# Kernel tuning notes

Measured on AMD Instinct MI355X. Metric: run time of the kernel, lower is better.

Reference implementation:

```python
import jax, jax.numpy as jnp
import numpy as np

EPS = 1e-5

def conv3x3(x, w, b):
    # x: [B,C,H,W], w: [O,I,3,3]
    y = jax.lax.conv_general_dilated(x, w, window_strides=(1, 1),
                                     padding=((1, 1), (1, 1)),
                                     dimension_numbers=('NCHW', 'OIHW', 'NCHW'))
    return y + b[None, :, None, None]

def batchnorm(x, gamma, beta):
    # training-mode BN: batch stats over (N,H,W), biased variance
    mean = jnp.mean(x, axis=(0, 2, 3), keepdims=True)
    var = jnp.mean((x - mean) ** 2, axis=(0, 2, 3), keepdims=True)
    xn = (x - mean) * jax.lax.rsqrt(var + EPS)
    return xn * gamma[None, :, None, None] + beta[None, :, None, None]

def setup_inputs() -> dict:
    key = jax.random.key(0)
    ks = jax.random.split(key, 5)
    B, C, H, W = 4, 256, 64, 64
    fan = C * 9
    return {
        'x': jax.random.normal(ks[0], (B, C, H, W), jnp.float32),
        'wv': jax.random.normal(ks[1], (C, C, 3, 3), jnp.float32) / np.sqrt(fan),
        'bv': jax.random.normal(ks[2], (C,), jnp.float32) * 0.01,
        'gv': jnp.ones((C,), jnp.float32),
        'betav': jnp.zeros((C,), jnp.float32),
        'ww': jax.random.normal(ks[3], (C, C, 3, 3), jnp.float32) / np.sqrt(fan),
        'bw': jax.random.normal(ks[4], (C,), jnp.float32) * 0.01,
        'gw': jnp.ones((C,), jnp.float32),
        'betaw': jnp.zeros((C,), jnp.float32),
    }

def reference(x, wv, bv, gv, betav, ww, bw, gw, betaw):
    B, C, H, W = x.shape
    N = H * W
    # value branch: conv3x3 + BN -> [B, N, C]
    value = batchnorm(conv3x3(x, wv, bv), gv, betav).reshape(B, C, N)
    key_ = x.reshape(B, C, N)              # [B, C, N]
    query = key_.transpose(0, 2, 1)        # [B, N, C]
    sim = jnp.einsum('bnc,bcm->bnm', query, key_) * (C ** -0.5)  # [B, N, N]
    sim = jax.nn.softmax(sim, axis=-1)
    context = jnp.einsum('bnm,bcm->bcn', sim, value)             # [B, C, N]
    context = context.reshape(B, C, H, W)
    out = jax.nn.relu(batchnorm(conv3x3(context, ww, bw), gw, betaw))
    return out
```

## Files before the change

### kernel.cpp

```cpp
#include <hip/hip_runtime.h>
#include <cstdint>
#include <cstddef>

typedef __attribute__((ext_vector_type(8))) __bf16 bf16x8;
typedef __attribute__((ext_vector_type(4))) __bf16 bf16x4;
typedef __attribute__((ext_vector_type(4))) float  f32x4;

#define NPIX 4096
#define CHN  256

__device__ __forceinline__ void async_copy16(void* lds, const void* g) {
  __builtin_amdgcn_global_load_lds(
      (const __attribute__((address_space(1))) unsigned int*)g,
      (__attribute__((address_space(3))) unsigned int*)lds, 16, 0, 0);
}

__global__ __launch_bounds__(256) void k_transpose_cast(
    const float* __restrict__ X, __bf16* __restrict__ xT)
{
  __shared__ float tile[64][65];
  const int bid = blockIdx.x;
  const int b  = bid >> 8;
  const int pt = (bid >> 2) & 63;
  const int ct = bid & 3;
  const int tid = threadIdx.x;
  const int tc = tid & 63, tr = tid >> 6;
  const float* Xb = X + ((size_t)b*CHN + ct*64)*NPIX + pt*64;
#pragma unroll
  for (int i=0;i<16;++i) {
    int row = tr + i*4;
    tile[row][tc] = Xb[(size_t)row*NPIX + tc];
  }
  __syncthreads();
  __bf16* Tb = xT + ((size_t)b*NPIX + pt*64)*CHN + ct*64;
#pragma unroll
  for (int i=0;i<16;++i) {
    int prow = tr + i*4;
    Tb[(size_t)prow*CHN + tc] = (__bf16)tile[tc][prow];
  }
}

__global__ __launch_bounds__(256) void k_wcast(
    const float* __restrict__ wv, const float* __restrict__ ww,
    __bf16* __restrict__ wvt, __bf16* __restrict__ wwt)
{
  int idx = blockIdx.x*256 + threadIdx.x;
  int t = idx >> 16;
  int o = (idx >> 8) & 255;
  int i = idx & 255;
  size_t src = ((size_t)o*256 + i)*9 + t;
  wvt[idx] = (__bf16)wv[src];
  wwt[idx] = (__bf16)ww[src];
}

__global__ __launch_bounds__(256, 2) void k_conv_tap(
    const __bf16* __restrict__ W9,
    const __bf16* __restrict__ Bt,
    const __bf16* __restrict__ zb,
    __bf16* __restrict__ Y)
{
  __shared__ __bf16 Alds[2][64*64];
  __shared__ __bf16 Blds[2][128*64];
  const int bid0 = blockIdx.x;
  const int bid = (bid0 & 7)*64 + (bid0 >> 3);
  const int b  = bid >> 7;
  const int mt = (bid >> 5) & 3;
  const int nt = bid & 31;
  const int m0 = mt << 6;
  const int p0 = nt << 7;
  const int tid = threadIdx.x;
  const int w = tid >> 6, l = tid & 63;
  const int l15 = l & 15, lhi = l >> 4;
  const int wr = (w >> 1) << 5;
  const int wc = (w & 1) << 6;

  const __bf16* Btb = Bt + ((size_t)b << 20);
  const f32x4 vzero = {0.f,0.f,0.f,0.f};
  f32x4 acc[2][4];
#pragma unroll
  for (int i=0;i<2;++i)
#pragma unroll
    for (int j=0;j<4;++j) acc[i][j] = vzero;

  auto stage = [&](int buf, int it) {
    const int t = it >> 2, kc = it & 3;
    const int dy = t/3 - 1, dx = t%3 - 1;
    const int dq = dy*64 + dx;
    const int k0 = kc << 6;
#pragma unroll
    for (int i=0;i<2;++i) {
      int inst = w*2 + i;
      int s = inst*64 + l;
      int row = s >> 3, ch = s & 7;
      const __bf16* g = W9 + (size_t)t*65536 + (size_t)(m0+row)*256 + k0
                        + ((ch ^ (row & 7)) << 3);
      async_copy16((char*)(&Alds[buf][0]) + inst*1024, g);
    }
#pragma unroll
    for (int i=0;i<4;++i) {
      int inst = w*4 + i;
      int s = inst*64 + l;
      int pp = s >> 3, ch = s & 7;
      int p = p0 + pp;
      int xx = (p & 63) + dx;
      int yy = (p >> 6) + dy;
      bool ok = ((unsigned)xx < 64u) & ((unsigned)yy < 64u);
      const __bf16* g = ok ? (Btb + (size_t)(p + dq)*256 + k0 + ((ch ^ (pp & 7)) << 3))
                           : zb;
      async_copy16((char*)(&Blds[buf][0]) + inst*1024, g);
    }
  };

  stage(0, 0);
#pragma unroll 1
  for (int it=0; it<36; ++it) {
    const int cur = it & 1;
    if (it < 35) {
      stage(cur^1, it+1);
      asm volatile("s_waitcnt vmcnt(6)" ::: "memory");
    } else {
      asm volatile("s_waitcnt vmcnt(0)" ::: "memory");
    }
    __builtin_amdgcn_s_barrier();
    __builtin_amdgcn_sched_barrier(0);

    const char* Ac = (const char*)(&Alds[cur][0]);
    const char* Bc = (const char*)(&Blds[cur][0]);
#pragma unroll
    for (int kk=0; kk<2; ++kk) {
      const int swz = (((kk<<2)+lhi) ^ (l15 & 7)) << 4;
      bf16x8 af[2], bfr[4];
#pragma unroll
      for (int i=0;i<2;++i)
        af[i] = *(const bf16x8*)(Ac + (size_t)(wr + 16*i + l15)*128 + swz);
#pragma unroll
      for (int j=0;j<4;++j)
        bfr[j] = *(const bf16x8*)(Bc + (size_t)(wc + 16*j + l15)*128 + swz);
#pragma unroll
      for (int i=0;i<2;++i)
#pragma unroll
        for (int j=0;j<4;++j)
          acc[i][j] = __builtin_amdgcn_mfma_f32_16x16x32_bf16(af[i], bfr[j], acc[i][j], 0,0,0);
    }
    __builtin_amdgcn_s_barrier();
  }

  __bf16* Yb = Y + ((size_t)b << 20);
#pragma unroll
  for (int i=0;i<2;++i)
#pragma unroll
    for (int j=0;j<4;++j)
#pragma unroll
      for (int r=0;r<4;++r) {
        int row = m0 + wr + 16*i + lhi*4 + r;
        int col = p0 + wc + 16*j + l15;
        Yb[(size_t)row*NPIX + col] = (__bf16)acc[i][j][r];
      }
}

__global__ __launch_bounds__(256) void k_bn_stats(
    const __bf16* __restrict__ Y, const float* __restrict__ gamma,
    const float* __restrict__ beta, float* __restrict__ scale,
    float* __restrict__ shift)
{
  const int c = blockIdx.x;
  const int tid = threadIdx.x;
  float s = 0.f, s2 = 0.f;
#pragma unroll 1
  for (int b=0;b<4;++b) {
    const __bf16* p = Y + ((size_t)b*CHN + c)*NPIX;
#pragma unroll
    for (int i=0;i<2;++i) {
      bf16x8 v = *(const bf16x8*)(p + (tid + i*256)*8);
#pragma unroll
      for (int j=0;j<8;++j) { float f = (float)v[j]; s += f; s2 += f*f; }
    }
  }
#pragma unroll
  for (int d=1; d<64; d<<=1) { s += __shfl_xor(s, d, 64); s2 += __shfl_xor(s2, d, 64); }
  __shared__ float rs[4], rs2[4];
  if ((tid & 63) == 0) { rs[tid>>6] = s; rs2[tid>>6] = s2; }
  __syncthreads();
  if (tid == 0) {
    float S  = rs[0]+rs[1]+rs[2]+rs[3];
    float S2 = rs2[0]+rs2[1]+rs2[2]+rs2[3];
    const float inv_n = 1.f/16384.f;
    float mean = S*inv_n;
    float var  = S2*inv_n - mean*mean;
    float rstd = rsqrtf(var + 1e-5f);
    float sc = gamma[c]*rstd;
    scale[c] = sc;
    shift[c] = beta[c] - mean*sc;
  }
}

__global__ __launch_bounds__(256) void k_bn_apply_bf16(
    const __bf16* __restrict__ Y, const float* __restrict__ scale,
    const float* __restrict__ shift, __bf16* __restrict__ V)
{
  size_t idx = ((size_t)blockIdx.x*256 + threadIdx.x)*8;
  int c = (int)((idx >> 12) & 255);
  bf16x8 v = *(const bf16x8*)(Y + idx);
  float sc = scale[c], sh = shift[c];
  bf16x8 r;
#pragma unroll
  for (int j=0;j<8;++j) r[j] = (__bf16)((float)v[j]*sc + sh);
  *(bf16x8*)(V + idx) = r;
}

__global__ __launch_bounds__(256) void k_bn_relu(
    const __bf16* __restrict__ Y, const float* __restrict__ scale,
    const float* __restrict__ shift, float* __restrict__ out)
{
  size_t idx = ((size_t)blockIdx.x*256 + threadIdx.x)*8;
  int c = (int)((idx >> 12) & 255);
  bf16x8 v = *(const bf16x8*)(Y + idx);
  float sc = scale[c], sh = shift[c];
  float4 r0, r1;
  r0.x = fmaxf((float)v[0]*sc + sh, 0.f);
  r0.y = fmaxf((float)v[1]*sc + sh, 0.f);
  r0.z = fmaxf((float)v[2]*sc + sh, 0.f);
  r0.w = fmaxf((float)v[3]*sc + sh, 0.f);
  r1.x = fmaxf((float)v[4]*sc + sh, 0.f);
  r1.y = fmaxf((float)v[5]*sc + sh, 0.f);
  r1.z = fmaxf((float)v[6]*sc + sh, 0.f);
  r1.w = fmaxf((float)v[7]*sc + sh, 0.f);
  *(float4*)(out + idx)     = r0;
  *(float4*)(out + idx + 4) = r1;
}

__global__ __launch_bounds__(512, 2) void k_attn(
    const __bf16* __restrict__ xT,
    const __bf16* __restrict__ val,
    __bf16* __restrict__ O)
{
  __shared__ __align__(16) char smem[141312];

  const int bid0 = blockIdx.x;
  const int bid = (bid0 & 7)*32 + (bid0 >> 3);
  const int b  = bid >> 6;
  const int q0 = (bid & 63) << 6;
  const int tid = threadIdx.x;
  const int w = tid >> 6, l = tid & 63;
  const int l15 = l & 15, lhi = l >> 4;
  const int qh  = w & 1;
  const int kvq = w >> 1;
  const int p   = kvq >> 1;
  const int cfh = kvq & 1;

  const __bf16* xTb = xT  + ((size_t)b << 20);
  const __bf16* vb  = val + ((size_t)b << 20);

  bf16x8 aq[2][8];
#pragma unroll
  for (int rg=0; rg<2; ++rg) {
    const __bf16* qp = xTb + (size_t)(q0 + qh*32 + rg*16 + l15)*256 + lhi*8;
#pragma unroll
    for (int kc=0; kc<8; ++kc) {
      bf16x8 v = *(const bf16x8*)(qp + kc*32);
#pragma unroll
      for (int j=0;j<8;++j) v[j] = (__bf16)((float)v[j] * 0.0625f);
      aq[rg][kc] = v;
    }
  }

  auto stage = [&](int buf, int m0) {
    char* kb = smem + buf*32768;
    char* vv = smem + 65536 + buf*32768;
#pragma unroll
    for (int i=0;i<4;++i) {
      int inst = w*4 + i;
      int s = inst*64 + l;
      int row = s >> 5, cs = s & 31;
      const __bf16* g = xTb + (size_t)(m0 + row)*256 + ((cs ^ (row & 7)) << 3);
      async_copy16(kb + inst*1024, g);
    }
#pragma unroll
    for (int i=0;i<4;++i) {
      int inst = w*4 + i;
      int s = inst*64 + l;
      int row = s >> 3, cs = s & 7;
      const __bf16* g = vb + (size_t)row*NPIX + m0 + ((cs ^ (row & 7)) << 3);
      async_copy16(vv + inst*1024, g);
    }
  };

  const f32x4 vzero = {0.f,0.f,0.f,0.f};
  float lsum[2][4];
#pragma unroll
  for (int rg=0;rg<2;++rg)
#pragma unroll
    for (int r=0;r<4;++r) lsum[rg][r] = 0.f;
  f32x4 o[2][8];
#pragma unroll
  for (int rg=0;rg<2;++rg)
#pragma unroll
    for (int cf=0; cf<8; ++cf) o[rg][cf] = vzero;

  stage(0, 0);

#pragma unroll 1
  for (int mt=0; mt<64; ++mt) {
    const int cur = mt & 1;
    asm volatile("s_waitcnt vmcnt(0)" ::: "memory");
    __builtin_amdgcn_s_barrier();
    __builtin_amdgcn_sched_barrier(0);
    if (mt < 63) stage(cur^1, (mt+1) << 6);

    const char* Kc = smem + cur*32768;
    const char* Vc = smem + 65536 + cur*32768;
    __bf16* pReg = (__bf16*)(smem + 131072 + (qh*2 + p)*2560);

    f32x4 s4[2];
    s4[0] = vzero; s4[1] = vzero;
    {
      const int krow = kvq*16 + l15;
      const char* kbase = Kc + krow*512;
#pragma unroll
      for (int kc=0; kc<8; ++kc) {
        bf16x8 bk = *(const bf16x8*)(kbase + ((((kc<<2)+lhi) ^ (krow&7)) << 4));
        s4[0] = __builtin_amdgcn_mfma_f32_16x16x32_bf16(aq[0][kc], bk, s4[0], 0,0,0);
        s4[1] = __builtin_amdgcn_mfma_f32_16x16x32_bf16(aq[1][kc], bk, s4[1], 0,0,0);
      }
    }

#pragma unroll
    for (int rg=0;rg<2;++rg)
#pragma unroll
      for (int r=0;r<4;++r) {
        float pv = __expf(s4[rg][r]);
        __bf16 pbf = (__bf16)pv;
        pReg[(rg*16 + lhi*4 + r)*40 + cfh*16 + l15] = pbf;
        lsum[rg][r] += (float)pbf;
      }

    asm volatile("s_waitcnt lgkmcnt(0)" ::: "memory");
    __builtin_amdgcn_s_barrier();
    __builtin_amdgcn_sched_barrier(0);

    bf16x8 pa0 = *(const bf16x8*)(pReg + (size_t)l15*40 + lhi*8);
    bf16x8 pa1 = *(const bf16x8*)(pReg + (size_t)(16 + l15)*40 + lhi*8);

#pragma unroll
    for (int cf=0; cf<8; ++cf) {
      const int c = cfh*128 + (cf<<4) + l15;
      const char* vbase = Vc + c*128;
      bf16x8 bv = *(const bf16x8*)(vbase + ((((p<<2)+lhi) ^ (c&7)) << 4));
      o[0][cf] = __builtin_amdgcn_mfma_f32_16x16x32_bf16(pa0, bv, o[0][cf], 0,0,0);
      o[1][cf] = __builtin_amdgcn_mfma_f32_16x16x32_bf16(pa1, bv, o[1][cf], 0,0,0);
    }
  }

#pragma unroll
  for (int rg=0;rg<2;++rg)
#pragma unroll
    for (int r=0;r<4;++r)
#pragma unroll
      for (int d=1; d<16; d<<=1) lsum[rg][r] += __shfl_xor(lsum[rg][r], d, 64);

  __builtin_amdgcn_s_barrier();
  float* oscr = (float*)smem;
  float* lscr = (float*)(smem + 65536);
  if (l15 == 0) {
#pragma unroll
    for (int rg=0;rg<2;++rg)
#pragma unroll
      for (int r=0;r<4;++r)
        lscr[w*32 + rg*16 + lhi*4 + r] = lsum[rg][r];
  }
  if (p == 1) {
    float* od = oscr + (size_t)(qh*2 + cfh)*4096;
#pragma unroll
    for (int rg=0;rg<2;++rg)
#pragma unroll
      for (int cf=0;cf<8;++cf)
#pragma unroll
        for (int r=0;r<4;++r)
          od[(rg*16 + lhi*4 + r)*128 + (cf<<4) + l15] = o[rg][cf][r];
  }
  asm volatile("s_waitcnt lgkmcnt(0)" ::: "memory");
  __builtin_amdgcn_s_barrier();
  if (p == 0) {
    const float* od = oscr + (size_t)(qh*2 + cfh)*4096;
    __bf16* Ob = O + ((size_t)b << 20);
#pragma unroll
    for (int rg=0;rg<2;++rg) {
      float inv[4];
#pragma unroll
      for (int r=0;r<4;++r) {
        float tot = 0.f;
#pragma unroll
        for (int k=0;k<4;++k)
          tot += lscr[(qh + 2*k)*32 + rg*16 + lhi*4 + r];
        inv[r] = 1.f / tot;
      }
#pragma unroll
      for (int cf=0;cf<8;++cf)
#pragma unroll
        for (int r=0;r<4;++r) {
          float vtot = o[rg][cf][r] + od[(rg*16 + lhi*4 + r)*128 + (cf<<4) + l15];
          int row = q0 + qh*32 + rg*16 + lhi*4 + r;
          Ob[(size_t)row*256 + cfh*128 + (cf<<4) + l15] = (__bf16)(vtot * inv[r]);
        }
    }
  }
}

extern "C" void kernel_launch(void* const* d_in, const int* in_sizes, int n_in,
                              void* d_out, int out_size, void* d_ws, size_t ws_size,
                              hipStream_t stream)
{
  const float* x     = (const float*)d_in[0];
  const float* wv    = (const float*)d_in[1];
  const float* gv    = (const float*)d_in[3];
  const float* betav = (const float*)d_in[4];
  const float* ww    = (const float*)d_in[5];
  const float* gw    = (const float*)d_in[7];
  const float* betaw = (const float*)d_in[8];
  float* out = (float*)d_out;

  char* ws = (char*)d_ws;
  __bf16* xT     = (__bf16*)(ws);
  __bf16* val    = (__bf16*)(ws + 8388608);
  __bf16* Obuf   = (__bf16*)(ws + 16777216);
  __bf16* ybuf   = (__bf16*)(ws + 25165824);
  __bf16* wvt    = (__bf16*)(ws + 33554432);
  __bf16* wwt    = (__bf16*)(ws + 34734080);
  float* scale_v = (float*)(ws + 35913728);
  float* shift_v = (float*)(ws + 35914752);
  float* scale_w = (float*)(ws + 35915776);
  float* shift_w = (float*)(ws + 35916800);
  __bf16* zbuf   = (__bf16*)(ws + 35917824);
  if (ws_size < 35918848) return;

  hipMemsetAsync(zbuf, 0, 1024, stream);

  k_transpose_cast<<<1024, 256, 0, stream>>>(x, xT);
  k_wcast<<<2304, 256, 0, stream>>>(wv, ww, wvt, wwt);

  k_conv_tap<<<512, 256, 0, stream>>>(wvt, xT, zbuf, ybuf);
  k_bn_stats<<<256, 256, 0, stream>>>(ybuf, gv, betav, scale_v, shift_v);
  k_bn_apply_bf16<<<2048, 256, 0, stream>>>(ybuf, scale_v, shift_v, val);

  k_attn<<<256, 512, 0, stream>>>(xT, val, Obuf);

  k_conv_tap<<<512, 256, 0, stream>>>(wwt, Obuf, zbuf, ybuf);
  k_bn_stats<<<256, 256, 0, stream>>>(ybuf, gw, betaw, scale_w, shift_w);
  k_bn_relu<<<2048, 256, 0, stream>>>(ybuf, scale_w, shift_w, out);
}
```

Measured before the change: 199.5 us.

## Load K and V tiles directly from global into registers, dropping LDS staging

Removes the double-buffered async LDS staging of K and V tiles in the attention kernel. Each wave now loads its K fragments and V fragments straight from global memory into registers, prefetching the next K tile after the barrier. The P-exchange buffer is double-buffered in a much smaller shared allocation, and the QK MFMA chain is split into two independent accumulators. This cuts LDS footprint and LDS traffic, but each wave now issues redundant, less coalesced global loads and relies on the cache, with V loads issued inside the loop without much latency hiding.

```diff
diff --git a/kernel.cpp b/kernel.cpp
--- a/kernel.cpp
+++ b/kernel.cpp
@@ -234,7 +234,7 @@
     const __bf16* __restrict__ val,
     __bf16* __restrict__ O)
 {
-  __shared__ __align__(16) char smem[141312];
+  __shared__ __align__(16) char smem[66560];
 
   const int bid0 = blockIdx.x;
   const int bid = (bid0 & 7)*32 + (bid0 >> 3);
@@ -264,27 +264,6 @@
     }
   }
 
-  auto stage = [&](int buf, int m0) {
-    char* kb = smem + buf*32768;
-    char* vv = smem + 65536 + buf*32768;
-#pragma unroll
-    for (int i=0;i<4;++i) {
-      int inst = w*4 + i;
-      int s = inst*64 + l;
-      int row = s >> 5, cs = s & 31;
-      const __bf16* g = xTb + (size_t)(m0 + row)*256 + ((cs ^ (row & 7)) << 3);
-      async_copy16(kb + inst*1024, g);
-    }
-#pragma unroll
-    for (int i=0;i<4;++i) {
-      int inst = w*4 + i;
-      int s = inst*64 + l;
-      int row = s >> 3, cs = s & 7;
-      const __bf16* g = vb + (size_t)row*NPIX + m0 + ((cs ^ (row & 7)) << 3);
-      async_copy16(vv + inst*1024, g);
-    }
-  };
-
   const f32x4 vzero = {0.f,0.f,0.f,0.f};
   float lsum[2][4];
 #pragma unroll
@@ -297,30 +276,40 @@
 #pragma unroll
     for (int cf=0; cf<8; ++cf) o[rg][cf] = vzero;
 
-  stage(0, 0);
+  bf16x8 kf[8];
+  {
+    const __bf16* kp = xTb + (size_t)(kvq*16 + l15)*256 + lhi*8;
+#pragma unroll
+    for (int kc=0;kc<8;++kc) kf[kc] = *(const bf16x8*)(kp + kc*32);
+  }
 
 #pragma unroll 1
   for (int mt=0; mt<64; ++mt) {
     const int cur = mt & 1;
-    asm volatile("s_waitcnt vmcnt(0)" ::: "memory");
-    __builtin_amdgcn_s_barrier();
-    __builtin_amdgcn_sched_barrier(0);
-    if (mt < 63) stage(cur^1, (mt+1) << 6);
-
-    const char* Kc = smem + cur*32768;
-    const char* Vc = smem + 65536 + cur*32768;
-    __bf16* pReg = (__bf16*)(smem + 131072 + (qh*2 + p)*2560);
-
+    __bf16* pReg = (__bf16*)(smem + cur*10240 + (qh*2 + p)*2560);
+
+    f32x4 sa0=vzero, sb0=vzero, sa1=vzero, sb1=vzero;
+#pragma unroll
+    for (int kc=0; kc<4; ++kc) {
+      sa0 = __builtin_amdgcn_mfma_f32_16x16x32_bf16(aq[0][kc], kf[kc], sa0, 0,0,0);
+      sa1 = __builtin_amdgcn_mfma_f32_16x16x32_bf16(aq[1][kc], kf[kc], sa1, 0,0,0);
+    }
+#pragma unroll
+    for (int kc=4; kc<8; ++kc) {
+      sb0 = __builtin_amdgcn_mfma_f32_16x16x32_bf16(aq[0][kc], kf[kc], sb0, 0,0,0);
+      sb1 = __builtin_amdgcn_mfma_f32_16x16x32_bf16(aq[1][kc], kf[kc], sb1, 0,0,0);
+    }
     f32x4 s4[2];
-    s4[0] = vzero; s4[1] = vzero;
+    s4[0] = sa0 + sb0;
+    s4[1] = sa1 + sb1;
+
+    bf16x8 vf[8];
     {
-      const int krow = kvq*16 + l15;
-      const char* kbase = Kc + krow*512;
-#pragma unroll
-      for (int kc=0; kc<8; ++kc) {
-        bf16x8 bk = *(const bf16x8*)(kbase + ((((kc<<2)+lhi) ^ (krow&7)) << 4));
-        s4[0] = __builtin_amdgcn_mfma_f32_16x16x32_bf16(aq[0][kc], bk, s4[0], 0,0,0);
-        s4[1] = __builtin_amdgcn_mfma_f32_16x16x32_bf16(aq[1][kc], bk, s4[1], 0,0,0);
+      const __bf16* vp = vb + (size_t)(mt*64 + p*32 + lhi*8);
+#pragma unroll
+      for (int cf=0;cf<8;++cf) {
+        int c = cfh*128 + (cf<<4) + l15;
+        vf[cf] = *(const bf16x8*)(vp + (size_t)c*NPIX);
       }
     }
 
@@ -338,16 +327,19 @@
     __builtin_amdgcn_s_barrier();
     __builtin_amdgcn_sched_barrier(0);
 
+    if (mt < 63) {
+      const __bf16* kp = xTb + (size_t)((mt+1)*64 + kvq*16 + l15)*256 + lhi*8;
+#pragma unroll
+      for (int kc=0;kc<8;++kc) kf[kc] = *(const bf16x8*)(kp + kc*32);
+    }
+
     bf16x8 pa0 = *(const bf16x8*)(pReg + (size_t)l15*40 + lhi*8);
     bf16x8 pa1 = *(const bf16x8*)(pReg + (size_t)(16 + l15)*40 + lhi*8);
 
 #pragma unroll
     for (int cf=0; cf<8; ++cf) {
-      const int c = cfh*128 + (cf<<4) + l15;
-      const char* vbase = Vc + c*128;
-      bf16x8 bv = *(const bf16x8*)(vbase + ((((p<<2)+lhi) ^ (c&7)) << 4));
-      o[0][cf] = __builtin_amdgcn_mfma_f32_16x16x32_bf16(pa0, bv, o[0][cf], 0,0,0);
-      o[1][cf] = __builtin_amdgcn_mfma_f32_16x16x32_bf16(pa1, bv, o[1][cf], 0,0,0);
+      o[0][cf] = __builtin_amdgcn_mfma_f32_16x16x32_bf16(pa0, vf[cf], o[0][cf], 0,0,0);
+      o[1][cf] = __builtin_amdgcn_mfma_f32_16x16x32_bf16(pa1, vf[cf], o[1][cf], 0,0,0);
     }
   }
 
```

Measured after the change: 331.2 us. 1.66x slower.
